# Kernel optimization log

Hardware: AMD Instinct MI355X
Metric: run time of the kernel (lower is better)

Reference implementation:

```python
import jax, jax.numpy as jnp
import numpy as np

B = 1024      # graphs
NODES = 128   # nodes per graph (uniform -> batch_ptr = arange(B+1)*NODES)
IN = 64
HID = 256
OUT = 128
NBLK = 3
TAU = 0.25


def _ln(x, g, b):
    # LayerNorm over last dim, eps=1e-5 (torch default)
    mu = jnp.mean(x, axis=-1, keepdims=True)
    var = jnp.mean((x - mu) ** 2, axis=-1, keepdims=True)
    return (x - mu) / jnp.sqrt(var + 1e-5) * g + b


def setup_inputs() -> dict:
    key = jax.random.key(0)
    ks = jax.random.split(key, 4)
    sc = 0.05
    return {
        "H": jax.random.normal(ks[0], (B * NODES, IN), jnp.float32),
        "batch_ptr": jnp.arange(B + 1, dtype=jnp.int32) * NODES,
        # ResNetMLP params: stem Linear(IN->HID)+LN, NBLK residual blocks
        # Linear(HID->HID)+LN+ReLU, head Linear(HID->OUT)+LN (last_norm=True).
        "W_in": jax.random.normal(ks[1], (IN, HID), jnp.float32) * sc,
        "b_in": jnp.zeros((HID,), jnp.float32),
        "g_in": jnp.ones((HID,), jnp.float32),
        "beta_in": jnp.zeros((HID,), jnp.float32),
        "Wb": jax.random.normal(ks[2], (NBLK, HID, HID), jnp.float32) * sc,
        "bb": jnp.zeros((NBLK, HID), jnp.float32),
        "gb": jnp.ones((NBLK, HID), jnp.float32),
        "betab": jnp.zeros((NBLK, HID), jnp.float32),
        "W_out": jax.random.normal(ks[3], (HID, OUT), jnp.float32) * sc,
        "b_out": jnp.zeros((OUT,), jnp.float32),
        "g_out": jnp.ones((OUT,), jnp.float32),
        "beta_out": jnp.zeros((OUT,), jnp.float32),
    }


def reference(H, batch_ptr, W_in, b_in, g_in, beta_in, Wb, bb, gb, betab,
              W_out, b_out, g_out, beta_out):
    # ResNetMLP projection (dropout is identity in eval)
    x = jax.nn.relu(_ln(H @ W_in + b_in, g_in, beta_in))          # [N, HID]
    for k in range(NBLK):
        x = x + jax.nn.relu(_ln(x @ Wb[k] + bb[k], gb[k], betab[k]))
    z = _ln(x @ W_out + b_out, g_out, beta_out)                   # [N, OUT]

    # Uniform-size graphs: ragged per-graph loop vectorizes to [Bg, n, OUT]
    Bg = batch_ptr.shape[0] - 1
    n = H.shape[0] // Bg
    z3 = z.reshape(Bg, n, OUT)

    # s_i = mean_j ||z_i - z_j||_2 (includes j=i, distance 0)
    sq = jnp.sum(z3 * z3, axis=-1)                                # [Bg, n]
    d2 = sq[:, :, None] + sq[:, None, :] - 2.0 * jnp.einsum("bid,bjd->bij", z3, z3)
    d = jnp.sqrt(jnp.maximum(d2, 0.0) + 1e-12)                    # [Bg, n, n]
    s = jnp.mean(d, axis=-1)                                      # [Bg, n]

    w = jax.nn.softmax(s / TAU, axis=-1)                          # [Bg, n]
    v_loc = jnp.einsum("bi,bid->bd", w, z3)                       # [Bg, OUT]
    return v_loc, w
```

## Files before the change

kernel.cpp:

```cpp
#include <hip/hip_runtime.h>
#include <stdint.h>


typedef __attribute__((ext_vector_type(8))) short bf16x8;
typedef __attribute__((ext_vector_type(4))) float f32x4;

#define XB_STRIDE 264
#define YB_STRIDE 260
#define ZB_STRIDE 136
#define LDS_YB    33792
#define LDS_PAR   100352
#define LDS_TOTAL 103424

__device__ __forceinline__ unsigned int rne16(float f) {
  unsigned int u = __builtin_bit_cast(unsigned int, f);
  return u + 0x7fffu + ((u >> 16) & 1u);
}
__device__ __forceinline__ unsigned short f2bf(float f) {
  return (unsigned short)(rne16(f) >> 16);
}
__device__ __forceinline__ float bf2f(unsigned short h) {
  unsigned int u = ((unsigned int)h) << 16;
  return __builtin_bit_cast(float, u);
}
__device__ __forceinline__ f32x4 zero4() {
  f32x4 v; v.x = 0.f; v.y = 0.f; v.z = 0.f; v.w = 0.f; return v;
}
template <int CTRL>
__device__ __forceinline__ float dpp_add(float v) {
  int p = __builtin_amdgcn_update_dpp(0, __builtin_bit_cast(int, v),
                                      CTRL, 0xF, 0xF, true);
  return v + __builtin_bit_cast(float, p);
}
__device__ __forceinline__ float red16(float v) {
  v = dpp_add<0xB1>(v);
  v = dpp_add<0x4E>(v);
  v = dpp_add<0x141>(v);
  v = dpp_add<0x140>(v);
  return v;
}

__global__ void prep_weights(const float* __restrict__ Win, const float* __restrict__ Wb,
                             const float* __restrict__ Wout, unsigned short* __restrict__ ws) {
  int g = blockIdx.x * 256 + threadIdx.x;
  if (g >= 30720) return;
  const float* W; int N; int local;
  if (g < 2048) { W = Win; N = 256; local = g; }
  else if (g < 26624) {
    int i = g - 2048; int blk = i >> 13; local = i & 8191;
    W = Wb + blk * 65536; N = 256;
  } else { W = Wout; N = 128; local = g - 26624; }
  int f = local >> 6, lane = local & 63;
  int NTL = N >> 4;
  int kc = f / NTL, ntile = f - kc * NTL;
  int n = ntile * 16 + (lane & 15);
  int k0 = kc * 32 + (lane >> 4) * 8;
  unsigned short o[8];
#pragma unroll
  for (int e = 0; e < 8; ++e) o[e] = f2bf(W[(size_t)(k0 + e) * N + n]);
  *reinterpret_cast<uint4*>(ws + (size_t)g * 8) = *reinterpret_cast<uint4*>(o);
}

template <int KL, int N, int MODE>
__device__ __forceinline__ void layer(unsigned short* __restrict__ Xb,
                                      float* __restrict__ Yb, float* __restrict__ par,
                                      const unsigned short* __restrict__ Wf,
                                      int tid, int wave, int lane,
                                      const float* __restrict__ bias,
                                      const float* __restrict__ gam,
                                      const float* __restrict__ bet,
                                      float (&xprev)[16],
                                      unsigned short* __restrict__ Z, size_t rowglob) {
  constexpr int NT = N / 128;
  constexpr int NTL = N / 16;
  constexpr int KC = KL / 32;
  constexpr int J = N / 64;
  const int wr = wave >> 3, wc = wave & 7;
  const int q = lane >> 4, l16 = lane & 15;
  const int rowbase = wr * 32;
  const int colbase = wc * 16 * NT;
  const unsigned short* Wl = Wf + lane * 8;

  f32x4 acc[2][NT];
#pragma unroll
  for (int mt = 0; mt < 2; ++mt)
#pragma unroll
    for (int nt = 0; nt < NT; ++nt) acc[mt][nt] = zero4();

  bf16x8 bcur[NT];
#pragma unroll
  for (int nt = 0; nt < NT; ++nt)
    bcur[nt] = *reinterpret_cast<const bf16x8*>(Wl + (size_t)(wc * NT + nt) * 512);

  __syncthreads();
  if (tid < 3 * N) {
    float v = (tid < N) ? bias[tid] : (tid < 2 * N) ? gam[tid - N] : bet[tid - 2 * N];
    par[tid] = v;
  }
#pragma unroll
  for (int kc = 0; kc < KC; ++kc) {
    bf16x8 bnext[NT];
    if (kc + 1 < KC) {
#pragma unroll
      for (int nt = 0; nt < NT; ++nt)
        bnext[nt] = *reinterpret_cast<const bf16x8*>(
            Wl + (size_t)((kc + 1) * NTL + wc * NT + nt) * 512);
    }
    const int kk = kc * 32 + q * 8;
    bf16x8 a0 = *reinterpret_cast<const bf16x8*>(Xb + (rowbase + l16) * XB_STRIDE + kk);
    bf16x8 a1 = *reinterpret_cast<const bf16x8*>(Xb + (rowbase + 16 + l16) * XB_STRIDE + kk);
#pragma unroll
    for (int nt = 0; nt < NT; ++nt)
      acc[0][nt] = __builtin_amdgcn_mfma_f32_16x16x32_bf16(a0, bcur[nt], acc[0][nt], 0, 0, 0);
#pragma unroll
    for (int nt = 0; nt < NT; ++nt)
      acc[1][nt] = __builtin_amdgcn_mfma_f32_16x16x32_bf16(a1, bcur[nt], acc[1][nt], 0, 0, 0);
    if (kc + 1 < KC) {
#pragma unroll
      for (int nt = 0; nt < NT; ++nt) bcur[nt] = bnext[nt];
    }
  }

#pragma unroll
  for (int mt = 0; mt < 2; ++mt)
#pragma unroll
    for (int nt = 0; nt < NT; ++nt) {
      const int col = colbase + 16 * nt + l16;
#pragma unroll
      for (int r = 0; r < 4; ++r)
        Yb[(rowbase + 16 * mt + 4 * q + r) * YB_STRIDE + col] = acc[mt][nt][r];
    }
  __syncthreads();

  const int row = wave * 4 + q;
  const int cb = l16 * 4;
  float y[4 * J];
#pragma unroll
  for (int j = 0; j < J; ++j)
    *reinterpret_cast<f32x4*>(y + 4 * j) =
        *reinterpret_cast<const f32x4*>(Yb + row * YB_STRIDE + cb + 64 * j);
  float bv[4 * J], gv[4 * J], ev[4 * J];
#pragma unroll
  for (int j = 0; j < J; ++j) {
    *reinterpret_cast<f32x4*>(bv + 4 * j) = *reinterpret_cast<const f32x4*>(par + cb + 64 * j);
    *reinterpret_cast<f32x4*>(gv + 4 * j) = *reinterpret_cast<const f32x4*>(par + N + cb + 64 * j);
    *reinterpret_cast<f32x4*>(ev + 4 * j) = *reinterpret_cast<const f32x4*>(par + 2 * N + cb + 64 * j);
  }
  float s1 = 0.f, s2 = 0.f;
#pragma unroll
  for (int e = 0; e < 4 * J; ++e) {
    y[e] += bv[e];
    s1 += y[e]; s2 = __builtin_fmaf(y[e], y[e], s2);
  }
  s1 = red16(s1); s2 = red16(s2);
  const float mu = s1 * (1.0f / N);
  const float var = s2 * (1.0f / N) - mu * mu;
  const float rstd = rsqrtf(var + 1e-5f);
  const float nmr = -mu * rstd;
#pragma unroll
  for (int j = 0; j < J; ++j) {
    unsigned int pk[2];
#pragma unroll
    for (int i = 0; i < 4; ++i) {
      const int e = 4 * j + i;
      float t = __builtin_fmaf(y[e], rstd, nmr);
      float o = __builtin_fmaf(t, gv[e], ev[e]);
      float xv;
      if constexpr (MODE == 0) { xv = fmaxf(o, 0.f); xprev[e] = xv; }
      else if constexpr (MODE == 1) { xv = xprev[e] + fmaxf(o, 0.f); xprev[e] = xv; }
      else { xv = o; }
      if (i & 1)
        pk[i >> 1] = __builtin_amdgcn_perm(rne16(xv),
                       rne16(__builtin_bit_cast(float, pk[i >> 1])), 0x07060302);
      else
        pk[i >> 1] = __builtin_bit_cast(unsigned int, xv);
    }
    if constexpr (MODE != 2) {
      unsigned int* Xw = reinterpret_cast<unsigned int*>(Xb);
      *reinterpret_cast<uint2*>(Xw + row * 132 + 2 * l16 + 32 * j) =
          *reinterpret_cast<uint2*>(pk);
    } else {
      *reinterpret_cast<uint2*>(Z + (rowglob + row) * 128 + cb + 64 * j) =
          *reinterpret_cast<uint2*>(pk);
    }
  }
}

__global__ __attribute__((amdgpu_flat_work_group_size(1024, 1024), amdgpu_waves_per_eu(4)))
void mlp_main(const float* __restrict__ H, const unsigned short* __restrict__ ws,
              const float* __restrict__ b_in, const float* __restrict__ g_in,
              const float* __restrict__ beta_in,
              const float* __restrict__ bb, const float* __restrict__ gb,
              const float* __restrict__ betab,
              const float* __restrict__ b_out, const float* __restrict__ g_out,
              const float* __restrict__ beta_out,
              unsigned short* __restrict__ Z) {
  extern __shared__ char smem[];
  unsigned short* Xb = (unsigned short*)smem;
  float* Yb = (float*)(smem + LDS_YB);
  float* par = (float*)(smem + LDS_PAR);
  const int tid = threadIdx.x;
  const int wave = tid >> 6, lane = tid & 63;
  const size_t rowglob = (size_t)blockIdx.x * 64;

  {
    int row = tid >> 4, c4 = (tid & 15) * 4;
    float4 f = *reinterpret_cast<const float4*>(H + (rowglob + row) * 64 + c4);
    uint2 o;
    o.x = __builtin_amdgcn_perm(rne16(f.y), rne16(f.x), 0x07060302);
    o.y = __builtin_amdgcn_perm(rne16(f.w), rne16(f.z), 0x07060302);
    *reinterpret_cast<uint2*>(Xb + row * XB_STRIDE + c4) = o;
  }

  float xprev[16];
  layer<64, 256, 0>(Xb, Yb, par, ws,           tid, wave, lane, b_in,     g_in,     beta_in,  xprev, Z, rowglob);
  layer<256, 256, 1>(Xb, Yb, par, ws + 16384,  tid, wave, lane, bb,       gb,       betab,    xprev, Z, rowglob);
  layer<256, 256, 1>(Xb, Yb, par, ws + 81920,  tid, wave, lane, bb + 256, gb + 256, betab + 256, xprev, Z, rowglob);
  layer<256, 256, 1>(Xb, Yb, par, ws + 147456, tid, wave, lane, bb + 512, gb + 512, betab + 512, xprev, Z, rowglob);
  layer<256, 128, 2>(Xb, Yb, par, ws + 212992, tid, wave, lane, b_out,    g_out,    beta_out, xprev, Z, rowglob);
}

__global__ __attribute__((amdgpu_flat_work_group_size(512, 512)))
void pool_main(const unsigned short* __restrict__ Z, float* __restrict__ out) {
  __shared__ unsigned short Zb[128 * ZB_STRIDE];
  __shared__ float sqv[128], sm[128], smw[128];
  const int tid = threadIdx.x;
  const int g = blockIdx.x;
  const int wave = tid >> 6, lane = tid & 63;
  const int q = lane >> 4, l16 = lane & 15;

  {
    int zr = tid >> 2, zc = (tid & 3) * 32;
    const uint4* zp = reinterpret_cast<const uint4*>(Z + ((size_t)g * 128 + zr) * 128 + zc);
    uint4* zd = reinterpret_cast<uint4*>(Zb + zr * ZB_STRIDE + zc);
    zd[0] = zp[0]; zd[1] = zp[1]; zd[2] = zp[2]; zd[3] = zp[3];
  }
  __syncthreads();

  f32x4 g2[8];
#pragma unroll
  for (int nt = 0; nt < 8; ++nt) g2[nt] = zero4();
#pragma unroll
  for (int ks = 0; ks < 4; ++ks) {
    int kk = ks * 32 + q * 8;
    bf16x8 a = *reinterpret_cast<const bf16x8*>(Zb + (16 * wave + l16) * ZB_STRIDE + kk);
#pragma unroll
    for (int nt = 0; nt < 8; ++nt) {
      bf16x8 bfr = *reinterpret_cast<const bf16x8*>(Zb + (16 * nt + l16) * ZB_STRIDE + kk);
      g2[nt] = __builtin_amdgcn_mfma_f32_16x16x32_bf16(a, bfr, g2[nt], 0, 0, 0);
    }
  }
  if ((l16 >> 2) == q) {
#pragma unroll
    for (int nt = 0; nt < 8; ++nt)
      if (nt == wave) {
#pragma unroll
        for (int r = 0; r < 4; ++r)
          if ((l16 & 3) == r) sqv[16 * wave + l16] = g2[nt][r];
      }
  }
  __syncthreads();
  float sqi[4];
#pragma unroll
  for (int r = 0; r < 4; ++r) sqi[r] = sqv[16 * wave + q * 4 + r];
  float sp[4] = {0.f, 0.f, 0.f, 0.f};
#pragma unroll
  for (int nt = 0; nt < 8; ++nt) {
    float sqj = sqv[16 * nt + l16];
#pragma unroll
    for (int r = 0; r < 4; ++r) {
      float d2 = sqi[r] + sqj - 2.0f * g2[nt][r];
      sp[r] += sqrtf(fmaxf(d2, 0.f) + 1e-12f);
    }
  }
#pragma unroll
  for (int d = 1; d < 16; d <<= 1) {
#pragma unroll
    for (int r = 0; r < 4; ++r) { float t = sp[r]; t += __shfl_xor(t, d); sp[r] = t; }
  }
  if (l16 == 0) {
#pragma unroll
    for (int r = 0; r < 4; ++r) sm[16 * wave + q * 4 + r] = sp[r] * (1.0f / 128.0f);
  }
  __syncthreads();
  if (wave == 0) {
    float l0 = sm[lane] * 4.0f;
    float l1 = sm[lane + 64] * 4.0f;
    float mx = fmaxf(l0, l1);
#pragma unroll
    for (int d = 1; d < 64; d <<= 1) mx = fmaxf(mx, __shfl_xor(mx, d));
    float e0 = __expf(l0 - mx), e1 = __expf(l1 - mx);
    float ss = e0 + e1;
#pragma unroll
    for (int d = 1; d < 64; d <<= 1) ss += __shfl_xor(ss, d);
    float inv = 1.0f / ss;
    float w0 = e0 * inv, w1 = e1 * inv;
    smw[lane] = w0;
    smw[lane + 64] = w1;
    out[131072 + g * 128 + lane] = w0;
    out[131072 + g * 128 + 64 + lane] = w1;
  }
  __syncthreads();
  {
    int c = 16 * wave + l16;
    float acv = 0.f;
#pragma unroll
    for (int i0 = 0; i0 < 32; ++i0) {
      int i = q * 32 + i0;
      acv += smw[i] * bf2f(Zb[i * ZB_STRIDE + c]);
    }
    acv += __shfl_xor(acv, 16);
    acv += __shfl_xor(acv, 32);
    if (q == 0) out[g * 128 + c] = acv;
  }
}

extern "C" void kernel_launch(void* const* d_in, const int* in_sizes, int n_in,
                              void* d_out, int out_size, void* d_ws, size_t ws_size,
                              hipStream_t stream) {
  (void)in_sizes; (void)n_in; (void)out_size; (void)ws_size;
  const float* H        = (const float*)d_in[0];
  const float* W_in     = (const float*)d_in[2];
  const float* b_in     = (const float*)d_in[3];
  const float* g_in     = (const float*)d_in[4];
  const float* beta_in  = (const float*)d_in[5];
  const float* Wb       = (const float*)d_in[6];
  const float* bb       = (const float*)d_in[7];
  const float* gb       = (const float*)d_in[8];
  const float* betab    = (const float*)d_in[9];
  const float* W_out    = (const float*)d_in[10];
  const float* b_out    = (const float*)d_in[11];
  const float* g_out    = (const float*)d_in[12];
  const float* beta_out = (const float*)d_in[13];
  float* out = (float*)d_out;
  unsigned short* ws = (unsigned short*)d_ws;
  unsigned short* Z = ws + 262144;

  prep_weights<<<120, 256, 0, stream>>>(W_in, Wb, W_out, ws);
  hipFuncSetAttribute(reinterpret_cast<const void*>(mlp_main),
                      hipFuncAttributeMaxDynamicSharedMemorySize, LDS_TOTAL);
  mlp_main<<<2048, 1024, LDS_TOTAL, stream>>>(H, ws, b_in, g_in, beta_in,
                                              bb, gb, betab, b_out, g_out, beta_out, Z);
  pool_main<<<1024, 512, 0, stream>>>(Z, out);
}
```

Baseline: 234.7 us.

## Retile MLP MFMA wave layout to 16-row strips and parallelize weight prep

Each of the 16 waves now owns a 16-row by 64-column output tile (4 waves down, 4 across) instead of 32 rows by 32 columns. Each wave therefore loads one A fragment per k-step and four B fragments, rather than two A and two B. This trades A-fragment reuse from LDS for more weight fragment loads from global or cache per wave. Separately, prep_weights now uses one thread per bf16 element, launched as 960 blocks, instead of one thread per 8-element vector. This raises parallelism in that kernel but gives up the 16-byte vector stores.

```diff
diff --git a/kernel.cpp b/kernel.cpp
--- a/kernel.cpp
+++ b/kernel.cpp
@@ -42,23 +42,20 @@
 
 __global__ void prep_weights(const float* __restrict__ Win, const float* __restrict__ Wb,
                              const float* __restrict__ Wout, unsigned short* __restrict__ ws) {
-  int g = blockIdx.x * 256 + threadIdx.x;
-  if (g >= 30720) return;
+  int t = blockIdx.x * 256 + threadIdx.x;
+  if (t >= 245760) return;
+  int g = t >> 3, e = t & 7;
   const float* W; int N; int local;
   if (g < 2048) { W = Win; N = 256; local = g; }
   else if (g < 26624) {
-    int i = g - 2048; int blk = i >> 13; local = i & 8191;
-    W = Wb + blk * 65536; N = 256;
+    int i = g - 2048; W = Wb + (i >> 13) * 65536; N = 256; local = i & 8191;
   } else { W = Wout; N = 128; local = g - 26624; }
   int f = local >> 6, lane = local & 63;
   int NTL = N >> 4;
   int kc = f / NTL, ntile = f - kc * NTL;
   int n = ntile * 16 + (lane & 15);
-  int k0 = kc * 32 + (lane >> 4) * 8;
-  unsigned short o[8];
-#pragma unroll
-  for (int e = 0; e < 8; ++e) o[e] = f2bf(W[(size_t)(k0 + e) * N + n]);
-  *reinterpret_cast<uint4*>(ws + (size_t)g * 8) = *reinterpret_cast<uint4*>(o);
+  int k = kc * 32 + ((lane >> 4) * 8) + e;
+  ws[t] = f2bf(W[(size_t)k * N + n]);
 }
 
 template <int KL, int N, int MODE>
@@ -71,21 +68,19 @@
                                       const float* __restrict__ bet,
                                       float (&xprev)[16],
                                       unsigned short* __restrict__ Z, size_t rowglob) {
-  constexpr int NT = N / 128;
+  constexpr int NT = N / 64;
   constexpr int NTL = N / 16;
   constexpr int KC = KL / 32;
   constexpr int J = N / 64;
-  const int wr = wave >> 3, wc = wave & 7;
+  const int wr = wave >> 2, wc = wave & 3;
   const int q = lane >> 4, l16 = lane & 15;
-  const int rowbase = wr * 32;
+  const int rowbase = wr * 16;
   const int colbase = wc * 16 * NT;
   const unsigned short* Wl = Wf + lane * 8;
 
-  f32x4 acc[2][NT];
-#pragma unroll
-  for (int mt = 0; mt < 2; ++mt)
-#pragma unroll
-    for (int nt = 0; nt < NT; ++nt) acc[mt][nt] = zero4();
+  f32x4 acc[NT];
+#pragma unroll
+  for (int nt = 0; nt < NT; ++nt) acc[nt] = zero4();
 
   bf16x8 bcur[NT];
 #pragma unroll
@@ -107,14 +102,10 @@
             Wl + (size_t)((kc + 1) * NTL + wc * NT + nt) * 512);
     }
     const int kk = kc * 32 + q * 8;
-    bf16x8 a0 = *reinterpret_cast<const bf16x8*>(Xb + (rowbase + l16) * XB_STRIDE + kk);
-    bf16x8 a1 = *reinterpret_cast<const bf16x8*>(Xb + (rowbase + 16 + l16) * XB_STRIDE + kk);
+    bf16x8 a = *reinterpret_cast<const bf16x8*>(Xb + (rowbase + l16) * XB_STRIDE + kk);
 #pragma unroll
     for (int nt = 0; nt < NT; ++nt)
-      acc[0][nt] = __builtin_amdgcn_mfma_f32_16x16x32_bf16(a0, bcur[nt], acc[0][nt], 0, 0, 0);
-#pragma unroll
-    for (int nt = 0; nt < NT; ++nt)
-      acc[1][nt] = __builtin_amdgcn_mfma_f32_16x16x32_bf16(a1, bcur[nt], acc[1][nt], 0, 0, 0);
+      acc[nt] = __builtin_amdgcn_mfma_f32_16x16x32_bf16(a, bcur[nt], acc[nt], 0, 0, 0);
     if (kc + 1 < KC) {
 #pragma unroll
       for (int nt = 0; nt < NT; ++nt) bcur[nt] = bnext[nt];
@@ -122,14 +113,12 @@
   }
 
 #pragma unroll
-  for (int mt = 0; mt < 2; ++mt)
-#pragma unroll
-    for (int nt = 0; nt < NT; ++nt) {
-      const int col = colbase + 16 * nt + l16;
-#pragma unroll
-      for (int r = 0; r < 4; ++r)
-        Yb[(rowbase + 16 * mt + 4 * q + r) * YB_STRIDE + col] = acc[mt][nt][r];
-    }
+  for (int nt = 0; nt < NT; ++nt) {
+    const int col = colbase + 16 * nt + l16;
+#pragma unroll
+    for (int r = 0; r < 4; ++r)
+      Yb[(rowbase + 4 * q + r) * YB_STRIDE + col] = acc[nt][r];
+  }
   __syncthreads();
 
   const int row = wave * 4 + q;
@@ -336,7 +325,7 @@
   unsigned short* ws = (unsigned short*)d_ws;
   unsigned short* Z = ws + 262144;
 
-  prep_weights<<<120, 256, 0, stream>>>(W_in, Wb, W_out, ws);
+  prep_weights<<<960, 256, 0, stream>>>(W_in, Wb, W_out, ws);
   hipFuncSetAttribute(reinterpret_cast<const void*>(mlp_main),
                       hipFuncAttributeMaxDynamicSharedMemorySize, LDS_TOTAL);
   mlp_main<<<2048, 1024, LDS_TOTAL, stream>>>(H, ws, b_in, g_in, beta_in,
```

Result: slower. 276.1 us (+17.6%).
